# Kernel optimization log

Hardware: AMD Instinct MI355X
Metric: run time of the kernel (lower is better)

## Reference

```python
import jax, jax.numpy as jnp
import numpy as np

B, H, KV, HD, D, S = 8, 32, 8, 128, 4096, 4096
PAST = S - 2  # 4094, cache nearly full
ROPE_THETA = 10000.0


def rotate_half(x):
    h = x.shape[-1] // 2
    return jnp.concatenate([-x[..., h:], x[..., :h]], axis=-1)


def setup_inputs() -> dict:
    key = jax.random.key(0)
    ks = jax.random.split(key, 10)
    hidden_states = jax.random.normal(ks[0], (B, 1, D), jnp.float32)
    # HF additive causal mask for decode: 0 where position is valid, -inf-ish beyond
    pos = jnp.arange(S)
    attention_mask = jnp.broadcast_to(
        jnp.where(pos < PAST + 1, 0.0, -1e9).astype(jnp.float32)[None, None, None, :],
        (B, 1, 1, S),
    )
    # RoPE cos/sin for the single decoded position (position id = PAST)
    inv_freq = 1.0 / (ROPE_THETA ** (jnp.arange(0, HD, 2, dtype=jnp.float32) / HD))
    ang = PAST * inv_freq  # [HD/2]
    emb = jnp.concatenate([ang, ang], axis=-1)  # [HD]
    cos = jnp.broadcast_to(jnp.cos(emb)[None, None, :], (B, 1, HD)).astype(jnp.float32)
    sin = jnp.broadcast_to(jnp.sin(emb)[None, None, :], (B, 1, HD)).astype(jnp.float32)
    past_key = jax.random.normal(ks[1], (B, KV, PAST, HD), jnp.float32)
    past_value = jax.random.normal(ks[2], (B, KV, PAST, HD), jnp.float32)
    k_cache = jax.random.normal(ks[3], (B, KV, S, HD), jnp.float32)
    v_cache = jax.random.normal(ks[4], (B, KV, S, HD), jnp.float32)
    Wq = jax.random.normal(ks[5], (D, H * HD), jnp.float32) * 0.02
    Wk = jax.random.normal(ks[6], (D, KV * HD), jnp.float32) * 0.02
    Wv = jax.random.normal(ks[7], (D, KV * HD), jnp.float32) * 0.02
    Wo = jax.random.normal(ks[8], (H * HD, D), jnp.float32) * 0.02
    return dict(hidden_states=hidden_states, attention_mask=attention_mask, cos=cos,
                sin=sin, past_key=past_key, past_value=past_value,
                k_cache=k_cache, v_cache=v_cache, Wq=Wq, Wk=Wk, Wv=Wv, Wo=Wo)


def reference(hidden_states, attention_mask, cos, sin, past_key, past_value,
              k_cache, v_cache, Wq, Wk, Wv, Wo):
    b = hidden_states.shape[0]
    past_len = past_key.shape[2]  # static
    # q/k/v projections for the single decode token
    q = (hidden_states @ Wq).reshape(b, 1, H, HD).transpose(0, 2, 1, 3)   # [B,H,1,hd]
    k = (hidden_states @ Wk).reshape(b, 1, KV, HD).transpose(0, 2, 1, 3)  # [B,KV,1,hd]
    v = (hidden_states @ Wv).reshape(b, 1, KV, HD).transpose(0, 2, 1, 3)
    # rotary: cos/sin [B,1,hd] -> unsqueeze head dim -> [B,1,1,hd]
    c = cos[:, None, :, :]
    s = sin[:, None, :, :]
    q = q * c + rotate_half(q) * s
    k = k * c + rotate_half(k) * s
    # StaticCache: scatter past K/V into positions [0, past_len), new token at past_len
    kf = k_cache.at[:, :, :past_len, :].set(past_key)
    kf = kf.at[:, :, past_len:past_len + 1, :].set(k)
    vf = v_cache.at[:, :, :past_len, :].set(past_value)
    vf = vf.at[:, :, past_len:past_len + 1, :].set(v)
    # GQA: repeat kv heads
    n_rep = H // KV
    kr = jnp.repeat(kf, n_rep, axis=1)  # [B,H,S,hd]
    vr = jnp.repeat(vf, n_rep, axis=1)
    scores = jnp.einsum('bhqd,bhkd->bhqk', q, kr) / np.float32(np.sqrt(HD))
    scores = scores + attention_mask  # [B,1,1,S] broadcasts over heads
    probs = jax.nn.softmax(scores.astype(jnp.float32), axis=-1).astype(q.dtype)
    out = jnp.einsum('bhqk,bhkd->bhqd', probs, vr)  # [B,H,1,hd]
    out = out.transpose(0, 2, 1, 3).reshape(b, 1, H * HD)
    return out @ Wo  # [B,1,D]
```

## Files before the change

kernel.cpp:

```cpp
#include <hip/hip_runtime.h>

#define BB 8
#define HH 32
#define KVH 8
#define HD 128
#define DD 4096
#define PAST 4094
#define QCOLS 4096
#define KVCOLS 1024
#define NC_QKV 6144
#define DCH 64
#define NDCH 64
#define CHUNK 64
#define NCHUNK 64

__global__ __launch_bounds__(256)
void matvec_partial(const float* __restrict__ hin,
                    const float* __restrict__ W0,
                    const float* __restrict__ W1,
                    const float* __restrict__ W2,
                    int c_w1, int c_w2, int NC,
                    float* __restrict__ part)
{
    __shared__ float hl[DCH][BB];
    const int tid = threadIdx.x;
    const int d0 = blockIdx.y * DCH;
    const int cb = blockIdx.x * 512;

    for (int idx = tid; idx < DCH * BB; idx += 256) {
        int dd = idx & (DCH - 1);
        int b = idx >> 6;
        hl[dd][b] = hin[b * DD + d0 + dd];
    }
    __syncthreads();

    const int c = cb + tid * 2;
    const float* W;
    int ldw, cl;
    if (c < c_w1)      { W = W0; ldw = c_w1;        cl = c; }
    else if (c < c_w2) { W = W1; ldw = c_w2 - c_w1; cl = c - c_w1; }
    else               { W = W2; ldw = NC - c_w2;   cl = c - c_w2; }
    const float* wp = W + (size_t)d0 * ldw + cl;

    float2 acc[BB];
    #pragma unroll
    for (int b = 0; b < BB; ++b) { acc[b].x = 0.f; acc[b].y = 0.f; }

    #pragma unroll 4
    for (int dd = 0; dd < DCH; ++dd) {
        float2 w = *(const float2*)wp;
        wp += ldw;
        float hv[8];
        *(float4*)&hv[0] = *(const float4*)&hl[dd][0];
        *(float4*)&hv[4] = *(const float4*)&hl[dd][4];
        #pragma unroll
        for (int b = 0; b < BB; ++b) {
            acc[b].x = fmaf(hv[b], w.x, acc[b].x);
            acc[b].y = fmaf(hv[b], w.y, acc[b].y);
        }
    }

    float* po = part + (size_t)blockIdx.y * (BB * NC) + c;
    #pragma unroll
    for (int b = 0; b < BB; ++b) {
        *(float2*)(po + (size_t)b * NC) = acc[b];
    }
}

__global__ __launch_bounds__(256)
void qkv_finish(const float* __restrict__ part,
                const float* __restrict__ cosv,
                const float* __restrict__ sinv,
                float* __restrict__ qout,
                float* __restrict__ knew,
                float* __restrict__ vnew)
{
    const int idx = blockIdx.x * 256 + threadIdx.x;
    const int b = idx / NC_QKV;
    const int c = idx - b * NC_QKV;

    const float* p = part + (size_t)b * NC_QKV + c;
    float s = 0.f;
    #pragma unroll 8
    for (int i = 0; i < NDCH; ++i) s += p[(size_t)i * (BB * NC_QKV)];

    if (c < QCOLS + KVCOLS) {
        const int hd = c & (HD - 1);
        const int partner = (hd < 64) ? (c + 64) : (c - 64);
        const float* pp = part + (size_t)b * NC_QKV + partner;
        float sp = 0.f;
        #pragma unroll 8
        for (int i = 0; i < NDCH; ++i) sp += pp[(size_t)i * (BB * NC_QKV)];
        const float cs = cosv[b * HD + hd];
        const float sn = sinv[b * HD + hd];
        const float r = (hd < 64) ? -sp : sp;
        const float val = fmaf(s, cs, r * sn);
        if (c < QCOLS) qout[b * QCOLS + c] = val * 0.08838834764831845f;
        else           knew[b * KVCOLS + (c - QCOLS)] = val;
    } else {
        vnew[b * KVCOLS + (c - QCOLS - KVCOLS)] = s;
    }
}

__global__ __launch_bounds__(64)
void attn_partial(const float* __restrict__ past_key,
                  const float* __restrict__ past_value,
                  const float* __restrict__ q,
                  const float* __restrict__ knew,
                  const float* __restrict__ vnew,
                  float* __restrict__ pacc,
                  float* __restrict__ pl)
{
    const int pair = blockIdx.x;
    const int chunk = blockIdx.y;
    const int b = pair >> 3;
    const int kv = pair & 7;
    const int lane = threadIdx.x;
    const int half = lane >> 5;
    const int lh = lane & 31;

    const float* qb = q + b * QCOLS + (kv * 4) * HD + 4 * lh;
    const float4 qv0 = *(const float4*)(qb);
    const float4 qv1 = *(const float4*)(qb + HD);
    const float4 qv2 = *(const float4*)(qb + 2 * HD);
    const float4 qv3 = *(const float4*)(qb + 3 * HD);

    const float* kb = past_key   + (size_t)pair * PAST * HD;
    const float* vb = past_value + (size_t)pair * PAST * HD;
    const float* kn = knew + pair * HD;
    const float* vn = vnew + pair * HD;

    float4 acc0 = {0,0,0,0}, acc1 = {0,0,0,0}, acc2 = {0,0,0,0}, acc3 = {0,0,0,0};
    float l0 = 0.f, l1 = 0.f, l2 = 0.f, l3 = 0.f;

    const int jbase = chunk * CHUNK + half;
    #pragma unroll 2
    for (int it = 0; it < 32; ++it) {
        const int j = jbase + it * 2;
        const bool valid = (j <= PAST);
        const float* kp;
        const float* vp;
        if (j < PAST) { kp = kb + (size_t)j * HD; vp = vb + (size_t)j * HD; }
        else          { kp = kn;                   vp = vn; }

        const float4 kk = *(const float4*)(kp + 4 * lh);
        float s0 = kk.x*qv0.x + kk.y*qv0.y + kk.z*qv0.z + kk.w*qv0.w;
        float s1 = kk.x*qv1.x + kk.y*qv1.y + kk.z*qv1.z + kk.w*qv1.w;
        float s2 = kk.x*qv2.x + kk.y*qv2.y + kk.z*qv2.z + kk.w*qv2.w;
        float s3 = kk.x*qv3.x + kk.y*qv3.y + kk.z*qv3.z + kk.w*qv3.w;

        #pragma unroll
        for (int m = 1; m <= 16; m <<= 1) {
            s0 += __shfl_xor(s0, m, 64);
            s1 += __shfl_xor(s1, m, 64);
            s2 += __shfl_xor(s2, m, 64);
            s3 += __shfl_xor(s3, m, 64);
        }

        const float4 vv = *(const float4*)(vp + 4 * lh);
        const float p0 = valid ? __expf(s0) : 0.f;
        const float p1 = valid ? __expf(s1) : 0.f;
        const float p2 = valid ? __expf(s2) : 0.f;
        const float p3 = valid ? __expf(s3) : 0.f;
        l0 += p0; l1 += p1; l2 += p2; l3 += p3;
        acc0.x = fmaf(p0, vv.x, acc0.x); acc0.y = fmaf(p0, vv.y, acc0.y);
        acc0.z = fmaf(p0, vv.z, acc0.z); acc0.w = fmaf(p0, vv.w, acc0.w);
        acc1.x = fmaf(p1, vv.x, acc1.x); acc1.y = fmaf(p1, vv.y, acc1.y);
        acc1.z = fmaf(p1, vv.z, acc1.z); acc1.w = fmaf(p1, vv.w, acc1.w);
        acc2.x = fmaf(p2, vv.x, acc2.x); acc2.y = fmaf(p2, vv.y, acc2.y);
        acc2.z = fmaf(p2, vv.z, acc2.z); acc2.w = fmaf(p2, vv.w, acc2.w);
        acc3.x = fmaf(p3, vv.x, acc3.x); acc3.y = fmaf(p3, vv.y, acc3.y);
        acc3.z = fmaf(p3, vv.z, acc3.z); acc3.w = fmaf(p3, vv.w, acc3.w);
    }

    l0 += __shfl_xor(l0, 32, 64);
    l1 += __shfl_xor(l1, 32, 64);
    l2 += __shfl_xor(l2, 32, 64);
    l3 += __shfl_xor(l3, 32, 64);
    acc0.x += __shfl_xor(acc0.x, 32, 64); acc0.y += __shfl_xor(acc0.y, 32, 64);
    acc0.z += __shfl_xor(acc0.z, 32, 64); acc0.w += __shfl_xor(acc0.w, 32, 64);
    acc1.x += __shfl_xor(acc1.x, 32, 64); acc1.y += __shfl_xor(acc1.y, 32, 64);
    acc1.z += __shfl_xor(acc1.z, 32, 64); acc1.w += __shfl_xor(acc1.w, 32, 64);
    acc2.x += __shfl_xor(acc2.x, 32, 64); acc2.y += __shfl_xor(acc2.y, 32, 64);
    acc2.z += __shfl_xor(acc2.z, 32, 64); acc2.w += __shfl_xor(acc2.w, 32, 64);
    acc3.x += __shfl_xor(acc3.x, 32, 64); acc3.y += __shfl_xor(acc3.y, 32, 64);
    acc3.z += __shfl_xor(acc3.z, 32, 64); acc3.w += __shfl_xor(acc3.w, 32, 64);

    if (half == 0) {
        float* po = pacc + (((size_t)pair * NCHUNK + chunk) * 4) * HD + 4 * lh;
        *(float4*)(po)          = acc0;
        *(float4*)(po + HD)     = acc1;
        *(float4*)(po + 2*HD)   = acc2;
        *(float4*)(po + 3*HD)   = acc3;
        if (lh == 0) {
            float* plo = pl + ((size_t)pair * NCHUNK + chunk) * 4;
            plo[0] = l0; plo[1] = l1; plo[2] = l2; plo[3] = l3;
        }
    }
}

__global__ __launch_bounds__(256)
void attn_combine(const float* __restrict__ pacc,
                  const float* __restrict__ pl,
                  float* __restrict__ attn_out)
{
    const int idx = blockIdx.x * 256 + threadIdx.x;
    const int d = idx & 127;
    const int h = (idx >> 7) & 31;
    const int b = idx >> 12;
    const int kv = h >> 2;
    const int qi = h & 3;
    const int pair = b * 8 + kv;

    const float* pa  = pacc + (((size_t)pair * NCHUNK) * 4 + qi) * HD + d;
    const float* pls = pl + (size_t)pair * NCHUNK * 4 + qi;
    float acc = 0.f, lsum = 0.f;
    #pragma unroll 8
    for (int c = 0; c < NCHUNK; ++c) {
        acc  += pa[(size_t)c * 4 * HD];
        lsum += pls[c * 4];
    }
    attn_out[b * QCOLS + h * HD + d] = acc / lsum;
}

__global__ __launch_bounds__(256)
void wo_finish(const float* __restrict__ part, float* __restrict__ out)
{
    const int idx = blockIdx.x * 256 + threadIdx.x;
    float s = 0.f;
    #pragma unroll 8
    for (int i = 0; i < NDCH; ++i) s += part[(size_t)i * (BB * QCOLS) + idx];
    out[idx] = s;
}

extern "C" void kernel_launch(void* const* d_in, const int* in_sizes, int n_in,
                              void* d_out, int out_size, void* d_ws, size_t ws_size,
                              hipStream_t stream)
{
    (void)in_sizes; (void)n_in; (void)out_size; (void)ws_size;
    const float* hidden     = (const float*)d_in[0];
    const float* cosv       = (const float*)d_in[2];
    const float* sinv       = (const float*)d_in[3];
    const float* past_key   = (const float*)d_in[4];
    const float* past_value = (const float*)d_in[5];
    const float* Wq = (const float*)d_in[8];
    const float* Wk = (const float*)d_in[9];
    const float* Wv = (const float*)d_in[10];
    const float* Wo = (const float*)d_in[11];
    float* out = (float*)d_out;
    float* ws  = (float*)d_ws;

    float* qkv_part = ws;
    float* qrope    = qkv_part + (size_t)NDCH * BB * NC_QKV;
    float* knew     = qrope + BB * QCOLS;
    float* vnew     = knew + BB * KVCOLS;
    float* pacc     = vnew + BB * KVCOLS;
    float* pl       = pacc + (size_t)64 * NCHUNK * 4 * HD;
    float* attn_out = pl + (size_t)64 * NCHUNK * 4;
    float* wo_part  = qkv_part;

    matvec_partial<<<dim3(12, NDCH), 256, 0, stream>>>(
        hidden, Wq, Wk, Wv, 4096, 5120, NC_QKV, qkv_part);
    qkv_finish<<<(BB * NC_QKV) / 256, 256, 0, stream>>>(
        qkv_part, cosv, sinv, qrope, knew, vnew);
    attn_partial<<<dim3(64, NCHUNK), 64, 0, stream>>>(
        past_key, past_value, qrope, knew, vnew, pacc, pl);
    attn_combine<<<(BB * HH * HD) / 256, 256, 0, stream>>>(pacc, pl, attn_out);
    matvec_partial<<<dim3(8, NDCH), 256, 0, stream>>>(
        attn_out, Wo, Wo, Wo, 4096, 5120, QCOLS, wo_part);
    wo_finish<<<(BB * QCOLS) / 256, 256, 0, stream>>>(wo_part, out);
}
```

Baseline: 111.3 us.

## Pair RoPE halves in qkv_finish, pack attention chunks per block, fast-path full chunks

```diff
diff --git a/kernel.cpp b/kernel.cpp
--- a/kernel.cpp
+++ b/kernel.cpp
@@ -13,6 +13,7 @@
 #define NDCH 64
 #define CHUNK 64
 #define NCHUNK 64
+#define QSCALE 0.08838834764831845f
 
 __global__ __launch_bounds__(256)
 void matvec_partial(const float* __restrict__ hin,
@@ -46,7 +47,7 @@
     #pragma unroll
     for (int b = 0; b < BB; ++b) { acc[b].x = 0.f; acc[b].y = 0.f; }
 
-    #pragma unroll 4
+    #pragma unroll 8
     for (int dd = 0; dd < DCH; ++dd) {
         float2 w = *(const float2*)wp;
         wp += ldw;
@@ -67,6 +68,7 @@
     }
 }
 
+#define FIN_PER_B 3584
 __global__ __launch_bounds__(256)
 void qkv_finish(const float* __restrict__ part,
                 const float* __restrict__ cosv,
@@ -76,33 +78,45 @@
                 float* __restrict__ vnew)
 {
     const int idx = blockIdx.x * 256 + threadIdx.x;
-    const int b = idx / NC_QKV;
-    const int c = idx - b * NC_QKV;
-
-    const float* p = part + (size_t)b * NC_QKV + c;
-    float s = 0.f;
-    #pragma unroll 8
-    for (int i = 0; i < NDCH; ++i) s += p[(size_t)i * (BB * NC_QKV)];
-
-    if (c < QCOLS + KVCOLS) {
-        const int hd = c & (HD - 1);
-        const int partner = (hd < 64) ? (c + 64) : (c - 64);
-        const float* pp = part + (size_t)b * NC_QKV + partner;
-        float sp = 0.f;
+    const int b = idx / FIN_PER_B;
+    const int r = idx - b * FIN_PER_B;
+
+    if (r < 2560) {
+        const int hd = r & 63;
+        const int head = r >> 6;
+        const int c_lo = head * HD + hd;
+        const float* p0 = part + (size_t)b * NC_QKV + c_lo;
+        const float* p1 = p0 + 64;
+        float s_lo = 0.f, s_hi = 0.f;
         #pragma unroll 8
-        for (int i = 0; i < NDCH; ++i) sp += pp[(size_t)i * (BB * NC_QKV)];
-        const float cs = cosv[b * HD + hd];
-        const float sn = sinv[b * HD + hd];
-        const float r = (hd < 64) ? -sp : sp;
-        const float val = fmaf(s, cs, r * sn);
-        if (c < QCOLS) qout[b * QCOLS + c] = val * 0.08838834764831845f;
-        else           knew[b * KVCOLS + (c - QCOLS)] = val;
+        for (int i = 0; i < NDCH; ++i) {
+            s_lo += p0[(size_t)i * (BB * NC_QKV)];
+            s_hi += p1[(size_t)i * (BB * NC_QKV)];
+        }
+        const float cs_lo = cosv[b * HD + hd];
+        const float sn_lo = sinv[b * HD + hd];
+        const float cs_hi = cosv[b * HD + hd + 64];
+        const float sn_hi = sinv[b * HD + hd + 64];
+        const float v_lo = fmaf(s_lo, cs_lo, -s_hi * sn_lo);
+        const float v_hi = fmaf(s_hi, cs_hi,  s_lo * sn_hi);
+        if (c_lo < QCOLS) {
+            qout[b * QCOLS + c_lo]      = v_lo * QSCALE;
+            qout[b * QCOLS + c_lo + 64] = v_hi * QSCALE;
+        } else {
+            knew[b * KVCOLS + (c_lo - QCOLS)]      = v_lo;
+            knew[b * KVCOLS + (c_lo - QCOLS) + 64] = v_hi;
+        }
     } else {
+        const int c = r - 2560 + QCOLS + KVCOLS;
+        const float* p = part + (size_t)b * NC_QKV + c;
+        float s = 0.f;
+        #pragma unroll 8
+        for (int i = 0; i < NDCH; ++i) s += p[(size_t)i * (BB * NC_QKV)];
         vnew[b * KVCOLS + (c - QCOLS - KVCOLS)] = s;
     }
 }
 
-__global__ __launch_bounds__(64)
+__global__ __launch_bounds__(256)
 void attn_partial(const float* __restrict__ past_key,
                   const float* __restrict__ past_value,
                   const float* __restrict__ q,
@@ -112,10 +126,11 @@
                   float* __restrict__ pl)
 {
     const int pair = blockIdx.x;
-    const int chunk = blockIdx.y;
+    const int wid = threadIdx.x >> 6;
+    const int chunk = blockIdx.y * 4 + wid;
     const int b = pair >> 3;
     const int kv = pair & 7;
-    const int lane = threadIdx.x;
+    const int lane = threadIdx.x & 63;
     const int half = lane >> 5;
     const int lh = lane & 31;
 
@@ -127,50 +142,83 @@
 
     const float* kb = past_key   + (size_t)pair * PAST * HD;
     const float* vb = past_value + (size_t)pair * PAST * HD;
-    const float* kn = knew + pair * HD;
-    const float* vn = vnew + pair * HD;
 
     float4 acc0 = {0,0,0,0}, acc1 = {0,0,0,0}, acc2 = {0,0,0,0}, acc3 = {0,0,0,0};
     float l0 = 0.f, l1 = 0.f, l2 = 0.f, l3 = 0.f;
 
     const int jbase = chunk * CHUNK + half;
-    #pragma unroll 2
-    for (int it = 0; it < 32; ++it) {
-        const int j = jbase + it * 2;
-        const bool valid = (j <= PAST);
-        const float* kp;
-        const float* vp;
-        if (j < PAST) { kp = kb + (size_t)j * HD; vp = vb + (size_t)j * HD; }
-        else          { kp = kn;                   vp = vn; }
-
-        const float4 kk = *(const float4*)(kp + 4 * lh);
-        float s0 = kk.x*qv0.x + kk.y*qv0.y + kk.z*qv0.z + kk.w*qv0.w;
-        float s1 = kk.x*qv1.x + kk.y*qv1.y + kk.z*qv1.z + kk.w*qv1.w;
-        float s2 = kk.x*qv2.x + kk.y*qv2.y + kk.z*qv2.z + kk.w*qv2.w;
-        float s3 = kk.x*qv3.x + kk.y*qv3.y + kk.z*qv3.z + kk.w*qv3.w;
-
-        #pragma unroll
-        for (int m = 1; m <= 16; m <<= 1) {
-            s0 += __shfl_xor(s0, m, 64);
-            s1 += __shfl_xor(s1, m, 64);
-            s2 += __shfl_xor(s2, m, 64);
-            s3 += __shfl_xor(s3, m, 64);
-        }
-
-        const float4 vv = *(const float4*)(vp + 4 * lh);
-        const float p0 = valid ? __expf(s0) : 0.f;
-        const float p1 = valid ? __expf(s1) : 0.f;
-        const float p2 = valid ? __expf(s2) : 0.f;
-        const float p3 = valid ? __expf(s3) : 0.f;
-        l0 += p0; l1 += p1; l2 += p2; l3 += p3;
-        acc0.x = fmaf(p0, vv.x, acc0.x); acc0.y = fmaf(p0, vv.y, acc0.y);
-        acc0.z = fmaf(p0, vv.z, acc0.z); acc0.w = fmaf(p0, vv.w, acc0.w);
-        acc1.x = fmaf(p1, vv.x, acc1.x); acc1.y = fmaf(p1, vv.y, acc1.y);
-        acc1.z = fmaf(p1, vv.z, acc1.z); acc1.w = fmaf(p1, vv.w, acc1.w);
-        acc2.x = fmaf(p2, vv.x, acc2.x); acc2.y = fmaf(p2, vv.y, acc2.y);
-        acc2.z = fmaf(p2, vv.z, acc2.z); acc2.w = fmaf(p2, vv.w, acc2.w);
-        acc3.x = fmaf(p3, vv.x, acc3.x); acc3.y = fmaf(p3, vv.y, acc3.y);
-        acc3.z = fmaf(p3, vv.z, acc3.z); acc3.w = fmaf(p3, vv.w, acc3.w);
+
+    if (chunk < NCHUNK - 1) {
+        const float* kp = kb + (size_t)jbase * HD + 4 * lh;
+        const float* vp = vb + (size_t)jbase * HD + 4 * lh;
+        #pragma unroll 4
+        for (int it = 0; it < 32; ++it) {
+            const float4 kk = *(const float4*)kp;  kp += 2 * HD;
+            float s0 = kk.x*qv0.x + kk.y*qv0.y + kk.z*qv0.z + kk.w*qv0.w;
+            float s1 = kk.x*qv1.x + kk.y*qv1.y + kk.z*qv1.z + kk.w*qv1.w;
+            float s2 = kk.x*qv2.x + kk.y*qv2.y + kk.z*qv2.z + kk.w*qv2.w;
+            float s3 = kk.x*qv3.x + kk.y*qv3.y + kk.z*qv3.z + kk.w*qv3.w;
+            #pragma unroll
+            for (int m = 1; m <= 16; m <<= 1) {
+                s0 += __shfl_xor(s0, m, 64);
+                s1 += __shfl_xor(s1, m, 64);
+                s2 += __shfl_xor(s2, m, 64);
+                s3 += __shfl_xor(s3, m, 64);
+            }
+            const float4 vv = *(const float4*)vp;  vp += 2 * HD;
+            const float p0 = __expf(s0);
+            const float p1 = __expf(s1);
+            const float p2 = __expf(s2);
+            const float p3 = __expf(s3);
+            l0 += p0; l1 += p1; l2 += p2; l3 += p3;
+            acc0.x = fmaf(p0, vv.x, acc0.x); acc0.y = fmaf(p0, vv.y, acc0.y);
+            acc0.z = fmaf(p0, vv.z, acc0.z); acc0.w = fmaf(p0, vv.w, acc0.w);
+            acc1.x = fmaf(p1, vv.x, acc1.x); acc1.y = fmaf(p1, vv.y, acc1.y);
+            acc1.z = fmaf(p1, vv.z, acc1.z); acc1.w = fmaf(p1, vv.w, acc1.w);
+            acc2.x = fmaf(p2, vv.x, acc2.x); acc2.y = fmaf(p2, vv.y, acc2.y);
+            acc2.z = fmaf(p2, vv.z, acc2.z); acc2.w = fmaf(p2, vv.w, acc2.w);
+            acc3.x = fmaf(p3, vv.x, acc3.x); acc3.y = fmaf(p3, vv.y, acc3.y);
+            acc3.z = fmaf(p3, vv.z, acc3.z); acc3.w = fmaf(p3, vv.w, acc3.w);
+        }
+    } else {
+        const float* kn = knew + pair * HD;
+        const float* vn = vnew + pair * HD;
+        #pragma unroll 2
+        for (int it = 0; it < 32; ++it) {
+            const int j = jbase + it * 2;
+            const bool valid = (j <= PAST);
+            const float* kp;
+            const float* vp;
+            if (j < PAST) { kp = kb + (size_t)j * HD; vp = vb + (size_t)j * HD; }
+            else          { kp = kn;                   vp = vn; }
+
+            const float4 kk = *(const float4*)(kp + 4 * lh);
+            float s0 = kk.x*qv0.x + kk.y*qv0.y + kk.z*qv0.z + kk.w*qv0.w;
+            float s1 = kk.x*qv1.x + kk.y*qv1.y + kk.z*qv1.z + kk.w*qv1.w;
+            float s2 = kk.x*qv2.x + kk.y*qv2.y + kk.z*qv2.z + kk.w*qv2.w;
+            float s3 = kk.x*qv3.x + kk.y*qv3.y + kk.z*qv3.z + kk.w*qv3.w;
+            #pragma unroll
+            for (int m = 1; m <= 16; m <<= 1) {
+                s0 += __shfl_xor(s0, m, 64);
+                s1 += __shfl_xor(s1, m, 64);
+                s2 += __shfl_xor(s2, m, 64);
+                s3 += __shfl_xor(s3, m, 64);
+            }
+            const float4 vv = *(const float4*)(vp + 4 * lh);
+            const float p0 = valid ? __expf(s0) : 0.f;
+            const float p1 = valid ? __expf(s1) : 0.f;
+            const float p2 = valid ? __expf(s2) : 0.f;
+            const float p3 = valid ? __expf(s3) : 0.f;
+            l0 += p0; l1 += p1; l2 += p2; l3 += p3;
+            acc0.x = fmaf(p0, vv.x, acc0.x); acc0.y = fmaf(p0, vv.y, acc0.y);
+            acc0.z = fmaf(p0, vv.z, acc0.z); acc0.w = fmaf(p0, vv.w, acc0.w);
+            acc1.x = fmaf(p1, vv.x, acc1.x); acc1.y = fmaf(p1, vv.y, acc1.y);
+            acc1.z = fmaf(p1, vv.z, acc1.z); acc1.w = fmaf(p1, vv.w, acc1.w);
+            acc2.x = fmaf(p2, vv.x, acc2.x); acc2.y = fmaf(p2, vv.y, acc2.y);
+            acc2.z = fmaf(p2, vv.z, acc2.z); acc2.w = fmaf(p2, vv.w, acc2.w);
+            acc3.x = fmaf(p3, vv.x, acc3.x); acc3.y = fmaf(p3, vv.y, acc3.y);
+            acc3.z = fmaf(p3, vv.z, acc3.z); acc3.w = fmaf(p3, vv.w, acc3.w);
+        }
     }
 
     l0 += __shfl_xor(l0, 32, 64);
@@ -261,9 +309,9 @@
 
     matvec_partial<<<dim3(12, NDCH), 256, 0, stream>>>(
         hidden, Wq, Wk, Wv, 4096, 5120, NC_QKV, qkv_part);
-    qkv_finish<<<(BB * NC_QKV) / 256, 256, 0, stream>>>(
+    qkv_finish<<<(BB * FIN_PER_B) / 256, 256, 0, stream>>>(
         qkv_part, cosv, sinv, qrope, knew, vnew);
-    attn_partial<<<dim3(64, NCHUNK), 64, 0, stream>>>(
+    attn_partial<<<dim3(64, NCHUNK / 4), 256, 0, stream>>>(
         past_key, past_value, qrope, knew, vnew, pacc, pl);
     attn_combine<<<(BB * HH * HD) / 256, 256, 0, stream>>>(pacc, pl, attn_out);
     matvec_partial<<<dim3(8, NDCH), 256, 0, stream>>>(
```

Result: no change. 111.7 us (+0.3%).
